# Kernel tuning notes

Hardware: AMD Instinct MI355X
Metric: run time of the kernel (lower is better)

Reference implementation:

```python
import jax, jax.numpy as jnp
import numpy as np

DIM = 1024
NUM_ATT = 8
NUM_HEADS = 16
HEAD_DIM = DIM // NUM_HEADS
ROPE_BASE = 10000.0
NEG_INF = -1e9


def _rope(x):
    # x: [B, H, L, hd]; torchtune-style interleaved RoPE applied along the sequence axis.
    B, H, L, hd = x.shape
    pos = jnp.arange(L, dtype=jnp.float32)
    inv_freq = 1.0 / (ROPE_BASE ** (jnp.arange(0, hd, 2, dtype=jnp.float32) / hd))
    ang = pos[:, None] * inv_freq[None, :]          # [L, hd/2]
    cos = jnp.cos(ang)[None, None]                  # [1,1,L,hd/2]
    sin = jnp.sin(ang)[None, None]
    xr = x.reshape(B, H, L, hd // 2, 2)
    x0, x1 = xr[..., 0], xr[..., 1]
    out = jnp.stack([x0 * cos - x1 * sin, x1 * cos + x0 * sin], axis=-1)
    return out.reshape(B, H, L, hd).astype(x.dtype)


def setup_inputs() -> dict:
    key = jax.random.key(0)
    ks = jax.random.split(key, 7)
    B, L = 32, 512
    x = jax.random.normal(ks[0], (B, L, DIM), dtype=jnp.float32)
    s = 0.02  # init scale for numerical sanity (init choice, not math)
    query_projs = jax.random.normal(ks[1], (NUM_ATT, DIM, DIM), dtype=jnp.float32) * s
    key_projs = jax.random.normal(ks[2], (NUM_ATT, DIM, DIM), dtype=jnp.float32) * s
    value_projs = jax.random.normal(ks[3], (NUM_ATT, DIM, DIM), dtype=jnp.float32) * s
    out_projs = jax.random.normal(ks[4], (NUM_ATT, DIM, DIM), dtype=jnp.float32) * s
    router_w = jax.random.normal(ks[5], (DIM, NUM_ATT), dtype=jnp.float32) * s
    router_b = jnp.zeros((NUM_ATT,), dtype=jnp.float32)
    return {"x": x, "query_projs": query_projs, "key_projs": key_projs,
            "value_projs": value_projs, "out_projs": out_projs,
            "router_w": router_w, "router_b": router_b}


def reference(x, query_projs, key_projs, value_projs, out_projs, router_w, router_b):
    B, L, D = x.shape
    H, hd = NUM_HEADS, HEAD_DIM
    scale = hd ** -0.5

    # top-1 routing on mean-pooled tokens
    logits = x.mean(axis=1) @ router_w + router_b       # [B, E]
    attn_probs = jax.nn.softmax(logits, axis=-1)
    routes = jnp.argmax(attn_probs, axis=-1)            # [B] int

    # per-batch weight gather (the memory-bound irregular access) + bmm
    qw = query_projs[routes]                             # [B, D, D]
    kw = key_projs[routes]
    vw = value_projs[routes]
    q = jnp.einsum('bld,bde->ble', x, qw)
    k = jnp.einsum('bld,bde->ble', x, kw)
    v = jnp.einsum('bld,bde->ble', x, vw)

    q = q.reshape(B, L, H, hd).transpose(0, 2, 1, 3)     # [B,H,L,hd]
    k = k.reshape(B, L, H, hd).transpose(0, 2, 1, 3)
    v = v.reshape(B, L, H, hd).transpose(0, 2, 1, 3)

    q = _rope(q)
    k = _rope(k)

    scores = jnp.einsum('bhld,bhmd->bhlm', q, k) * scale  # [B,H,L,L]
    causal = jnp.triu(jnp.ones((L, L), dtype=bool), k=1)  # True above diag = masked
    scores = jnp.where(causal[None, None], NEG_INF, scores)
    attn = jax.nn.softmax(scores, axis=-1)
    out = jnp.einsum('bhlm,bhmd->bhld', attn, v)          # [B,H,L,hd]
    out = out.transpose(0, 2, 1, 3).reshape(B, L, D)

    ow = out_projs[routes]                                # [B, D, D]
    out = jnp.einsum('bld,bde->ble', out, ow)
    return out, attn_probs
```

## Files before the change

### kernel.cpp

```cpp
#include <hip/hip_runtime.h>


typedef __attribute__((ext_vector_type(8))) short bf16x8;
typedef __attribute__((ext_vector_type(4))) float f32x4;

typedef const __attribute__((address_space(1))) unsigned short* gas_t;
typedef __attribute__((address_space(3))) unsigned short* las_t;

#define OFF_PART   (0ull)
#define OFF_ROUTES (2ull << 20)
#define OFF_XB     (3ull << 20)
#define OFF_WT     (40ull << 20)
#define OFF_QKV    (112ull << 20)

__device__ __forceinline__ unsigned short f2bf(float f){
  unsigned int u = __float_as_uint(f);
  u += 0x7fffu + ((u >> 16) & 1u);
  return (unsigned short)(u >> 16);
}


__global__ void meanpool_kernel(const float* __restrict__ x, float* __restrict__ part,
                                unsigned short* __restrict__ xb){
  const int b = blockIdx.x, lc = blockIdx.y, t = threadIdx.x;
  const size_t base = ((size_t)b*512 + lc*32)*1024;
  const float* xs = x + base;
  unsigned short* xo = xb + base;
  float4 a = {0.f, 0.f, 0.f, 0.f};
  for (int l = 0; l < 32; ++l){
    const float4 v = *(const float4*)(xs + l*1024 + t*4);
    a.x += v.x; a.y += v.y; a.z += v.z; a.w += v.w;
    ushort4 pk;
    pk.x = f2bf(v.x); pk.y = f2bf(v.y); pk.z = f2bf(v.z); pk.w = f2bf(v.w);
    *(ushort4*)(xo + l*1024 + t*4) = pk;
  }
  *(float4*)(part + ((size_t)b*16 + lc)*1024 + t*4) = a;
}


__global__ void router_kernel(const float* __restrict__ part,
                              const float* __restrict__ rw,
                              const float* __restrict__ rbias,
                              float* __restrict__ probs,
                              int* __restrict__ routes){
  const int b = blockIdx.x, t = threadIdx.x;
  const int lane = t & 63, wave = t >> 6;
  __shared__ float wred[4][8];
  float p[8] = {0.f,0.f,0.f,0.f,0.f,0.f,0.f,0.f};
  #pragma unroll
  for (int k = 0; k < 4; ++k){
    const int d = t + k*256;
    float s = 0.f;
    #pragma unroll
    for (int lc = 0; lc < 16; ++lc)
      s += part[((size_t)b*16 + lc)*1024 + d];
    s *= (1.0f/512.0f);
    const float4 w0 = *(const float4*)(rw + d*8);
    const float4 w1 = *(const float4*)(rw + d*8 + 4);
    p[0] = fmaf(s, w0.x, p[0]); p[1] = fmaf(s, w0.y, p[1]);
    p[2] = fmaf(s, w0.z, p[2]); p[3] = fmaf(s, w0.w, p[3]);
    p[4] = fmaf(s, w1.x, p[4]); p[5] = fmaf(s, w1.y, p[5]);
    p[6] = fmaf(s, w1.z, p[6]); p[7] = fmaf(s, w1.w, p[7]);
  }
  #pragma unroll
  for (int off = 1; off < 64; off <<= 1)
    #pragma unroll
    for (int e = 0; e < 8; ++e)
      p[e] += __shfl_xor(p[e], off, 64);
  if (lane == 0){
    #pragma unroll
    for (int e = 0; e < 8; ++e) wred[wave][e] = p[e];
  }
  __syncthreads();
  if (t == 0){
    float lg[8], mx = -3e38f; int am = 0;
    #pragma unroll
    for (int e = 0; e < 8; ++e){
      lg[e] = wred[0][e] + wred[1][e] + wred[2][e] + wred[3][e] + rbias[e];
      if (lg[e] > mx){ mx = lg[e]; am = e; }
    }
    float sum = 0.f, ex[8];
    #pragma unroll
    for (int e = 0; e < 8; ++e){ ex[e] = __expf(lg[e] - mx); sum += ex[e]; }
    const float inv = 1.0f / sum;
    #pragma unroll
    for (int e = 0; e < 8; ++e) probs[b*8 + e] = ex[e] * inv;
    routes[b] = am;
  }
}


__global__ void wcast_kernel(const float* __restrict__ W, unsigned short* __restrict__ Wt){
  __shared__ float tile[64][65];
  const int mtx = blockIdx.z;
  const float* Wm = W + (size_t)mtx*1024*1024;
  unsigned short* Wo = Wt + (size_t)mtx*1024*1024;
  const int t = threadIdx.x;
  const int r = t >> 4;
  const int c4 = t & 15;
  const int gx = blockIdx.x*64, gy = blockIdx.y*64;
  #pragma unroll
  for (int k = 0; k < 4; ++k){
    const int rr = r + 16*k;
    const float4 v = *(const float4*)(Wm + (size_t)(gy + rr)*1024 + gx + c4*4);
    tile[rr][c4*4+0] = v.x; tile[rr][c4*4+1] = v.y;
    tile[rr][c4*4+2] = v.z; tile[rr][c4*4+3] = v.w;
  }
  __syncthreads();
  #pragma unroll
  for (int k = 0; k < 4; ++k){
    const int rr = r + 16*k;
    ushort4 pk;
    pk.x = f2bf(tile[c4*4+0][rr]); pk.y = f2bf(tile[c4*4+1][rr]);
    pk.z = f2bf(tile[c4*4+2][rr]); pk.w = f2bf(tile[c4*4+3][rr]);
    *(ushort4*)(Wo + (size_t)(gx + rr)*1024 + gy + c4*4) = pk;
  }
}


template<int MODE>
__global__ __launch_bounds__(512, 2) void gemm_kernel(
    const unsigned short* __restrict__ A,
    const unsigned short* __restrict__ Wt,
    const int* __restrict__ routes,
    unsigned short* __restrict__ qkvout,
    float* __restrict__ outf)
{
  __shared__ __align__(16) unsigned short As[2][256*64];
  __shared__ __align__(16) unsigned short Bs[2][256*64];

  const int f = blockIdx.x + blockIdx.y*8;
  const int CH = (MODE == 0) ? 96 : 32;
  const int wg = (f & 7)*CH + (f >> 3);
  const int slice = wg >> 3;
  const int tile  = wg & 7;
  const int m0 = (tile >> 2)*256;
  const int n0 = (tile & 3)*256;
  const int b = (MODE == 0) ? (slice/3) : slice;
  const int p = (MODE == 0) ? (slice - b*3) : 0;

  const int route = routes[b];
  const unsigned short* Ab = A + (size_t)b*512*1024;
  const unsigned short* Wb = Wt + (size_t)((MODE == 0) ? (p*8 + route) : route)*1024*1024;

  const int t = threadIdx.x;
  const int lane = t & 63;
  const int wave = t >> 6;
  const int wm = (wave >> 2)*128;
  const int wn = (wave & 3)*64;
  const int quad = lane >> 4;
  const int ln = lane & 15;

  const int srow = t >> 3;
  const int sch  = (t & 7) ^ (srow & 7);
  const unsigned short* gA0 = Ab + (size_t)(m0 + srow)*1024 + sch*8;
  const unsigned short* gB0 = Wb + (size_t)(n0 + srow)*1024 + sch*8;

  const int w8 = ln & 7;
  const int aO0 = (wm + ln)*64 + ((quad    ) ^ w8)*8;
  const int aO1 = (wm + ln)*64 + ((quad + 4) ^ w8)*8;
  const int bO0 = (wn + ln)*64 + ((quad    ) ^ w8)*8;
  const int bO1 = (wn + ln)*64 + ((quad + 4) ^ w8)*8;

  f32x4 acc[8][4] = {};
  bf16x8 a0[4][2], a1[4][2], b01[2][2], b23[2][2];

#define STAGE(c_, T_) do { \
    const size_t ko_ = (size_t)(T_)*64; \
    las_t dA_ = (las_t)(&As[c_][0]) + (size_t)t*8; \
    las_t dB_ = (las_t)(&Bs[c_][0]) + (size_t)t*8; \
    _Pragma("unroll") \
    for (int k_ = 0; k_ < 4; ++k_){ \
      __builtin_amdgcn_global_load_lds((gas_t)(gA0 + ko_ + (size_t)k_*65536), dA_ + k_*4096, 16, 0, 0); \
      __builtin_amdgcn_global_load_lds((gas_t)(gB0 + ko_ + (size_t)k_*65536), dB_ + k_*4096, 16, 0, 0); \
    } \
  } while (0)

#define RD(ptr_, off_) (*(const bf16x8*)((ptr_) + (off_)))
#define READ_F0(pA_, pB_) do { \
    _Pragma("unroll") for (int f_ = 0; f_ < 4; ++f_){ \
      a0[f_][0] = RD(pA_, aO0 + f_*1024); a0[f_][1] = RD(pA_, aO1 + f_*1024); } \
    _Pragma("unroll") for (int f_ = 0; f_ < 2; ++f_){ \
      b01[f_][0] = RD(pB_, bO0 + f_*1024); b01[f_][1] = RD(pB_, bO1 + f_*1024); } \
  } while (0)
#define READ_F1(pA_) do { \
    _Pragma("unroll") for (int f_ = 0; f_ < 4; ++f_){ \
      a1[f_][0] = RD(pA_, aO0 + (4+f_)*1024); a1[f_][1] = RD(pA_, aO1 + (4+f_)*1024); } \
  } while (0)
#define READ_F2(pB_) do { \
    _Pragma("unroll") for (int f_ = 0; f_ < 2; ++f_){ \
      b23[f_][0] = RD(pB_, bO0 + (2+f_)*1024); b23[f_][1] = RD(pB_, bO1 + (2+f_)*1024); } \
  } while (0)

#define MSET(AF_, BF_, IB_, JB_) do { \
    _Pragma("unroll") for (int f_ = 0; f_ < 4; ++f_) \
    _Pragma("unroll") for (int n_ = 0; n_ < 2; ++n_) \
    _Pragma("unroll") for (int k_ = 0; k_ < 2; ++k_) \
      acc[IB_+f_][JB_+n_] = __builtin_amdgcn_mfma_f32_16x16x32_bf16( \
          AF_[f_][k_], BF_[n_][k_], acc[IB_+f_][JB_+n_], 0, 0, 0); \
  } while (0)

  STAGE(0, 0);
  STAGE(1, 1);
  asm volatile("s_waitcnt vmcnt(8)" ::: "memory");
  __builtin_amdgcn_s_barrier();
  READ_F0((&As[0][0]), (&Bs[0][0]));

  for (int g = 0; g < 16; ++g){
    const int c = g & 1;
    const unsigned short* pA  = &As[c][0];
    const unsigned short* pB  = &Bs[c][0];
    const unsigned short* pAn = &As[c ^ 1][0];
    const unsigned short* pBn = &Bs[c ^ 1][0];

    READ_F1(pA);
    __builtin_amdgcn_s_barrier();
    asm volatile("s_waitcnt lgkmcnt(8)" ::: "memory");
    __builtin_amdgcn_sched_barrier(0);
    __builtin_amdgcn_s_setprio(1);
    MSET(a0, b01, 0, 0);
    __builtin_amdgcn_s_setprio(0);
    __builtin_amdgcn_s_barrier();

    READ_F2(pB);
    __builtin_amdgcn_s_barrier();
    asm volatile("s_waitcnt lgkmcnt(4)" ::: "memory");
    __builtin_amdgcn_sched_barrier(0);
    __builtin_amdgcn_s_setprio(1);
    MSET(a1, b01, 4, 0);
    __builtin_amdgcn_s_setprio(0);
    __builtin_amdgcn_s_barrier();

    asm volatile("s_waitcnt lgkmcnt(0)" ::: "memory");
    __builtin_amdgcn_sched_barrier(0);
    __builtin_amdgcn_s_setprio(1);
    MSET(a1, b23, 4, 2);
    __builtin_amdgcn_s_setprio(0);
    __builtin_amdgcn_s_barrier();

    if (g < 14){
      STAGE(c, g + 2);
      asm volatile("s_waitcnt vmcnt(8)" ::: "memory");
    } else if (g == 14){
      asm volatile("s_waitcnt vmcnt(0)" ::: "memory");
    }
    __builtin_amdgcn_s_barrier();
    __builtin_amdgcn_s_setprio(1);
    MSET(a0, b23, 0, 2);
    __builtin_amdgcn_s_setprio(0);
    if (g < 15) READ_F0(pAn, pBn);
    __builtin_amdgcn_s_barrier();
  }
#undef STAGE
#undef RD
#undef READ_F0
#undef READ_F1
#undef READ_F2
#undef MSET

  if (MODE == 0){
    const size_t PSZ = (size_t)32*16*512*64;
    if (p < 2){
      #pragma unroll
      for (int fn = 0; fn < 4; ++fn){
        const int e  = n0 + wn + fn*16 + ln;
        const int h  = e >> 6;
        const int eh = e & 63;
        const float invf = exp2f(-0.41524101f * (float)(eh >> 1));
        float s1, c1; __sincosf(invf, &s1, &c1);
        unsigned short* outp = qkvout + ((((size_t)p*32 + b)*16 + h)*512)*64 + eh;
        #pragma unroll
        for (int fm = 0; fm < 8; ++fm){
          const int l0 = m0 + wm + fm*16 + quad*4;
          float sn, cs;
          __sincosf((float)l0 * invf, &sn, &cs);
          #pragma unroll
          for (int r = 0; r < 4; ++r){
            const int l = l0 + r;
            const float own = acc[fm][fn][r];
            const float par = __shfl_xor(own, 1, 64);
            const float v = (e & 1) ? fmaf(own, cs, par*sn) : fmaf(own, cs, -par*sn);
            outp[(size_t)l*64] = f2bf(v);
            const float nc = cs*c1 - sn*s1;
            const float ns = sn*c1 + cs*s1;
            cs = nc; sn = ns;
          }
        }
      }
    } else {
      #pragma unroll
      for (int fn = 0; fn < 4; ++fn){
        const int e  = n0 + wn + fn*16 + ln;
        const int h  = e >> 6;
        const int eh = e & 63;
        unsigned short* outp = qkvout + 2*PSZ + (((size_t)b*16 + h)*64 + eh)*512;
        #pragma unroll
        for (int fm = 0; fm < 8; ++fm){
          const int l0 = m0 + wm + fm*16 + quad*4;
          ushort4 pk;
          pk.x = f2bf(acc[fm][fn][0]); pk.y = f2bf(acc[fm][fn][1]);
          pk.z = f2bf(acc[fm][fn][2]); pk.w = f2bf(acc[fm][fn][3]);
          *(ushort4*)(outp + l0) = pk;
        }
      }
    }
  } else {
    #pragma unroll
    for (int fn = 0; fn < 4; ++fn){
      const int e = n0 + wn + fn*16 + ln;
      #pragma unroll
      for (int fm = 0; fm < 8; ++fm){
        #pragma unroll
        for (int r = 0; r < 4; ++r){
          const int l = m0 + wm + fm*16 + quad*4 + r;
          outf[((size_t)b*512 + l)*1024 + e] = acc[fm][fn][r];
        }
      }
    }
  }
}


#define PSTR 72

__global__ __launch_bounds__(256, 3) void attn_kernel(
    const unsigned short* __restrict__ qkv,
    unsigned short* __restrict__ ctx)
{
  __shared__ __align__(16) unsigned short Ks[2][64*64];
  __shared__ __align__(16) unsigned short Vts[2][64*64];
  __shared__ __align__(16) unsigned short Ps[4][32*PSTR];

  int wg = blockIdx.x + (blockIdx.y << 2) + (blockIdx.z << 6);
  wg = (wg & 7) * 256 + (wg >> 3);
  const int b  = wg >> 6;
  const int h  = (wg >> 2) & 15;
  const int qt = wg & 3;

  const size_t HO  = (((size_t)b)*16 + h)*512*64;
  const size_t PSZ = (size_t)32*16*512*64;
  const unsigned short* Qg  = qkv + HO;
  const unsigned short* Kg  = qkv + PSZ + HO;
  const unsigned short* Vtg = qkv + 2*PSZ + HO;

  const int t    = threadIdx.x;
  const int lane = t & 63;
  const int wave = t >> 6;
  const int quad = lane >> 4;
  const int ln   = lane & 15;

  const int u0 = t, u1 = t + 256;
  const int kr0 = u0 >> 3, kc0 = (u0 & 7) ^ (kr0 & 7);
  const int kr1 = u1 >> 3, kc1 = (u1 & 7) ^ (kr1 & 7);

  bf16x8 aq[2][2];
  #pragma unroll
  for (int rg = 0; rg < 2; ++rg){
    const int row = qt*128 + rg*64 + wave*16 + ln;
    #pragma unroll
    for (int ks = 0; ks < 2; ++ks)
      aq[rg][ks] = *(const bf16x8*)(Qg + (size_t)row*64 + ks*32 + quad*8);
  }

  const int ktEnd = 2*qt + 1;

  __builtin_amdgcn_global_load_lds((gas_t)(Kg  + kr0*64  + kc0*8), (las_t)(Ks[0]  + u0*8), 16,0,0);
  __builtin_amdgcn_global_load_lds((gas_t)(Kg  + kr1*64  + kc1*8), (las_t)(Ks[0]  + u1*8), 16,0,0);
  __builtin_amdgcn_global_load_lds((gas_t)(Vtg + kr0*512 + kc0*8), (las_t)(Vts[0] + u0*8), 16,0,0);
  __builtin_amdgcn_global_load_lds((gas_t)(Vtg + kr1*512 + kc1*8), (las_t)(Vts[0] + u1*8), 16,0,0);

  float m_r[2][4], l_r[2][4];
  #pragma unroll
  for (int rg = 0; rg < 2; ++rg)
    #pragma unroll
    for (int r = 0; r < 4; ++r){ m_r[rg][r] = -3e38f; l_r[rg][r] = 0.f; }
  f32x4 o[2][4] = {};

  const int swzl = ln & 7;
  unsigned short* Pw = Ps[wave];
  const int rowoff = wave*16 + quad*4;

  for (int kt = 0; kt <= ktEnd; ++kt){
    __syncthreads();
    if (kt < ktEnd){
      const unsigned short* Kn  = Kg + (kt+1)*4096;
      const int col = (kt+1)*64;
      unsigned short* kb = Ks[(kt+1)&1];
      unsigned short* vb = Vts[(kt+1)&1];
      __builtin_amdgcn_global_load_lds((gas_t)(Kn  + kr0*64 + kc0*8),        (las_t)(kb + u0*8), 16,0,0);
      __builtin_amdgcn_global_load_lds((gas_t)(Kn  + kr1*64 + kc1*8),        (las_t)(kb + u1*8), 16,0,0);
      __builtin_amdgcn_global_load_lds((gas_t)(Vtg + kr0*512 + col + kc0*8), (las_t)(vb + u0*8), 16,0,0);
      __builtin_amdgcn_global_load_lds((gas_t)(Vtg + kr1*512 + col + kc1*8), (las_t)(vb + u1*8), 16,0,0);
    }
    const unsigned short* ks_ = Ks[kt&1];
    const unsigned short* vt_ = Vts[kt&1];

    #pragma unroll
    for (int rg = 0; rg < 2; ++rg){
      if (rg == 0 && kt > 2*qt) continue;
      const bool diag = (kt == 2*qt + rg);

      f32x4 s[4] = {};
      __builtin_amdgcn_s_setprio(1);
      #pragma unroll
      for (int ks2 = 0; ks2 < 2; ++ks2){
        #pragma unroll
        for (int kn = 0; kn < 4; ++kn){
          const bf16x8 bk = *(const bf16x8*)(ks_ + (kn*16+ln)*64 + (((quad + ks2*4) ^ swzl))*8);
          s[kn] = __builtin_amdgcn_mfma_f32_16x16x32_bf16(aq[rg][ks2], bk, s[kn], 0, 0, 0);
        }
      }
      __builtin_amdgcn_s_setprio(0);

      float p[4][4], lm[4] = {-3e38f,-3e38f,-3e38f,-3e38f};
      #pragma unroll
      for (int kn = 0; kn < 4; ++kn){
        const int col = kn*16 + ln;
        #pragma unroll
        for (int r = 0; r < 4; ++r){
          float v = s[kn][r] * 0.125f;
          if (diag && col > rowoff + r) v = -1e9f;
          p[kn][r] = v;
          lm[r] = fmaxf(lm[r], v);
        }
      }
      #pragma unroll
      for (int off = 1; off < 16; off <<= 1)
        #pragma unroll
        for (int r = 0; r < 4; ++r)
          lm[r] = fmaxf(lm[r], __shfl_xor(lm[r], off, 64));
      float alpha[4], rsum[4];
      #pragma unroll
      for (int r = 0; r < 4; ++r){
        const float mn = fmaxf(m_r[rg][r], lm[r]);
        alpha[r] = __expf(m_r[rg][r] - mn);
        m_r[rg][r] = mn;
      }
      #pragma unroll
      for (int kn = 0; kn < 4; ++kn)
        #pragma unroll
        for (int r = 0; r < 4; ++r)
          p[kn][r] = __expf(p[kn][r] - m_r[rg][r]);
      #pragma unroll
      for (int r = 0; r < 4; ++r)
        rsum[r] = (p[0][r] + p[1][r]) + (p[2][r] + p[3][r]);
      #pragma unroll
      for (int off = 1; off < 16; off <<= 1)
        #pragma unroll
        for (int r = 0; r < 4; ++r)
          rsum[r] += __shfl_xor(rsum[r], off, 64);
      #pragma unroll
      for (int r = 0; r < 4; ++r) l_r[rg][r] = l_r[rg][r]*alpha[r] + rsum[r];
      #pragma unroll
      for (int dn = 0; dn < 4; ++dn)
        #pragma unroll
        for (int r = 0; r < 4; ++r)
          o[rg][dn][r] *= alpha[r];

      #pragma unroll
      for (int kn = 0; kn < 4; ++kn)
        #pragma unroll
        for (int r = 0; r < 4; ++r)
          Pw[(rg*16 + quad*4 + r)*PSTR + kn*16 + ln] = f2bf(p[kn][r]);

      __builtin_amdgcn_s_setprio(1);
      #pragma unroll
      for (int ks2 = 0; ks2 < 2; ++ks2){
        const bf16x8 ap = *(const bf16x8*)(Pw + (rg*16 + ln)*PSTR + quad*8 + ks2*32);
        #pragma unroll
        for (int dn = 0; dn < 4; ++dn){
          const bf16x8 bv = *(const bf16x8*)(vt_ + (dn*16+ln)*64 + (((quad + ks2*4) ^ swzl))*8);
          o[rg][dn] = __builtin_amdgcn_mfma_f32_16x16x32_bf16(ap, bv, o[rg][dn], 0, 0, 0);
        }
      }
      __builtin_amdgcn_s_setprio(0);
    }
  }

  #pragma unroll
  for (int rg = 0; rg < 2; ++rg){
    #pragma unroll
    for (int r = 0; r < 4; ++r){
      const float inv = 1.0f / l_r[rg][r];
      const int row = qt*128 + rg*64 + wave*16 + quad*4 + r;
      unsigned short* op = ctx + ((size_t)b*512 + row)*1024 + h*64 + ln;
      #pragma unroll
      for (int dn = 0; dn < 4; ++dn)
        op[dn*16] = f2bf(o[rg][dn][r] * inv);
    }
  }
}


extern "C" void kernel_launch(void* const* d_in, const int* in_sizes, int n_in,
                              void* d_out, int out_size, void* d_ws, size_t ws_size,
                              hipStream_t stream) {
  const float* x     = (const float*)d_in[0];
  const float* qw    = (const float*)d_in[1];
  const float* kw    = (const float*)d_in[2];
  const float* vw    = (const float*)d_in[3];
  const float* ow    = (const float*)d_in[4];
  const float* rw    = (const float*)d_in[5];
  const float* rbias = (const float*)d_in[6];
  float* out = (float*)d_out;
  char* ws = (char*)d_ws;

  float* part            = (float*)(ws + OFF_PART);
  int* routes            = (int*)(ws + OFF_ROUTES);
  unsigned short* xb     = (unsigned short*)(ws + OFF_XB);
  unsigned short* wt     = (unsigned short*)(ws + OFF_WT);
  unsigned short* qkvbuf = (unsigned short*)(ws + OFF_QKV);
  unsigned short* ctx    = xb;
  float* probs = out + (size_t)32*512*1024;

  meanpool_kernel<<<dim3(32, 16), 256, 0, stream>>>(x, part, xb);
  router_kernel<<<32, 256, 0, stream>>>(part, rw, rbias, probs, routes);
  wcast_kernel<<<dim3(16, 16, 8), 256, 0, stream>>>(qw, wt);
  wcast_kernel<<<dim3(16, 16, 8), 256, 0, stream>>>(kw, wt + (size_t)8*1024*1024);
  wcast_kernel<<<dim3(16, 16, 8), 256, 0, stream>>>(vw, wt + (size_t)16*1024*1024);
  wcast_kernel<<<dim3(16, 16, 8), 256, 0, stream>>>(ow, wt + (size_t)24*1024*1024);
  gemm_kernel<0><<<dim3(8, 96), 512, 0, stream>>>(xb, wt, routes, qkvbuf, nullptr);
  attn_kernel<<<dim3(4, 16, 32), 256, 0, stream>>>(qkvbuf, ctx);
  gemm_kernel<1><<<dim3(8, 32), 512, 0, stream>>>(ctx, wt + (size_t)24*1024*1024, routes,
                                                  nullptr, out);
}
```

Before: 513.6 us.

## Permute GEMM B-tile columns so each lane owns four adjacent outputs for vector stores

Remaps which output columns each lane's MFMA fragments cover, so a lane holds four consecutive columns (ln*4+fn) instead of columns strided by 16. The B-tile LDS swizzle and read offsets change to match. The epilogues can then apply RoPE pairs within one thread without cross-lane shuffles, and can write packed ushort4 and float4 stores instead of scalar strided ones. The cost is a different LDS bank-conflict pattern on B reads, which needs the new swizzle to stay conflict-free.

```diff
diff --git a/kernel.cpp b/kernel.cpp
--- a/kernel.cpp
+++ b/kernel.cpp
@@ -152,15 +152,16 @@
   const int ln = lane & 15;
 
   const int srow = t >> 3;
-  const int sch  = (t & 7) ^ (srow & 7);
-  const unsigned short* gA0 = Ab + (size_t)(m0 + srow)*1024 + sch*8;
-  const unsigned short* gB0 = Wb + (size_t)(n0 + srow)*1024 + sch*8;
+  const int schA = (t & 7) ^ (srow & 7);
+  const int schB = (t & 7) ^ ((t >> 5) & 7);
+  const unsigned short* gA0 = Ab + (size_t)(m0 + srow)*1024 + schA*8;
+  const unsigned short* gB0 = Wb + (size_t)(n0 + srow)*1024 + schB*8;
 
   const int w8 = ln & 7;
   const int aO0 = (wm + ln)*64 + ((quad    ) ^ w8)*8;
   const int aO1 = (wm + ln)*64 + ((quad + 4) ^ w8)*8;
-  const int bO0 = (wn + ln)*64 + ((quad    ) ^ w8)*8;
-  const int bO1 = (wn + ln)*64 + ((quad + 4) ^ w8)*8;
+  const int bO0 = (wn + ln*4)*64 + ((quad    ) ^ w8)*8;
+  const int bO1 = (wn + ln*4)*64 + ((quad + 4) ^ w8)*8;
 
   f32x4 acc[8][4] = {};
   bf16x8 a0[4][2], a1[4][2], b01[2][2], b23[2][2];
@@ -181,7 +182,7 @@
     _Pragma("unroll") for (int f_ = 0; f_ < 4; ++f_){ \
       a0[f_][0] = RD(pA_, aO0 + f_*1024); a0[f_][1] = RD(pA_, aO1 + f_*1024); } \
     _Pragma("unroll") for (int f_ = 0; f_ < 2; ++f_){ \
-      b01[f_][0] = RD(pB_, bO0 + f_*1024); b01[f_][1] = RD(pB_, bO1 + f_*1024); } \
+      b01[f_][0] = RD(pB_, bO0 + f_*64); b01[f_][1] = RD(pB_, bO1 + f_*64); } \
   } while (0)
 #define READ_F1(pA_) do { \
     _Pragma("unroll") for (int f_ = 0; f_ < 4; ++f_){ \
@@ -189,7 +190,7 @@
   } while (0)
 #define READ_F2(pB_) do { \
     _Pragma("unroll") for (int f_ = 0; f_ < 2; ++f_){ \
-      b23[f_][0] = RD(pB_, bO0 + (2+f_)*1024); b23[f_][1] = RD(pB_, bO1 + (2+f_)*1024); } \
+      b23[f_][0] = RD(pB_, bO0 + (2+f_)*64); b23[f_][1] = RD(pB_, bO1 + (2+f_)*64); } \
   } while (0)
 
 #define MSET(AF_, BF_, IB_, JB_) do { \
@@ -260,39 +261,41 @@
 
   if (MODE == 0){
     const size_t PSZ = (size_t)32*16*512*64;
+    const int h = (n0 + wn) >> 6;
     if (p < 2){
+      const int eh0 = ln*4;
+      const float invf0 = exp2f(-0.41524101f * (float)(ln*2));
+      const float invf1 = invf0 * 0.74989420832f;
+      float sc0, cc0, sc1, cc1;
+      __sincosf(invf0, &sc0, &cc0);
+      __sincosf(invf1, &sc1, &cc1);
+      unsigned short* outp = qkvout + ((((size_t)p*32 + b)*16 + h)*512)*64 + eh0;
+      #pragma unroll
+      for (int fm = 0; fm < 8; ++fm){
+        const int l0 = m0 + wm + fm*16 + quad*4;
+        float s0, c0, s1, c1;
+        __sincosf((float)l0 * invf0, &s0, &c0);
+        __sincosf((float)l0 * invf1, &s1, &c1);
+        #pragma unroll
+        for (int r = 0; r < 4; ++r){
+          const int l = l0 + r;
+          const float x0 = acc[fm][0][r], x1 = acc[fm][1][r];
+          const float x2 = acc[fm][2][r], x3 = acc[fm][3][r];
+          ushort4 pk;
+          pk.x = f2bf(x0*c0 - x1*s0);
+          pk.y = f2bf(x1*c0 + x0*s0);
+          pk.z = f2bf(x2*c1 - x3*s1);
+          pk.w = f2bf(x3*c1 + x2*s1);
+          *(ushort4*)(outp + (size_t)l*64) = pk;
+          const float nc0 = c0*cc0 - s0*sc0, ns0 = s0*cc0 + c0*sc0;
+          const float nc1 = c1*cc1 - s1*sc1, ns1 = s1*cc1 + c1*sc1;
+          c0 = nc0; s0 = ns0; c1 = nc1; s1 = ns1;
+        }
+      }
+    } else {
       #pragma unroll
       for (int fn = 0; fn < 4; ++fn){
-        const int e  = n0 + wn + fn*16 + ln;
-        const int h  = e >> 6;
-        const int eh = e & 63;
-        const float invf = exp2f(-0.41524101f * (float)(eh >> 1));
-        float s1, c1; __sincosf(invf, &s1, &c1);
-        unsigned short* outp = qkvout + ((((size_t)p*32 + b)*16 + h)*512)*64 + eh;
-        #pragma unroll
-        for (int fm = 0; fm < 8; ++fm){
-          const int l0 = m0 + wm + fm*16 + quad*4;
-          float sn, cs;
-          __sincosf((float)l0 * invf, &sn, &cs);
-          #pragma unroll
-          for (int r = 0; r < 4; ++r){
-            const int l = l0 + r;
-            const float own = acc[fm][fn][r];
-            const float par = __shfl_xor(own, 1, 64);
-            const float v = (e & 1) ? fmaf(own, cs, par*sn) : fmaf(own, cs, -par*sn);
-            outp[(size_t)l*64] = f2bf(v);
-            const float nc = cs*c1 - sn*s1;
-            const float ns = sn*c1 + cs*s1;
-            cs = nc; sn = ns;
-          }
-        }
-      }
-    } else {
-      #pragma unroll
-      for (int fn = 0; fn < 4; ++fn){
-        const int e  = n0 + wn + fn*16 + ln;
-        const int h  = e >> 6;
-        const int eh = e & 63;
+        const int eh = ln*4 + fn;
         unsigned short* outp = qkvout + 2*PSZ + (((size_t)b*16 + h)*64 + eh)*512;
         #pragma unroll
         for (int fm = 0; fm < 8; ++fm){
@@ -305,16 +308,16 @@
       }
     }
   } else {
-    #pragma unroll
-    for (int fn = 0; fn < 4; ++fn){
-      const int e = n0 + wn + fn*16 + ln;
-      #pragma unroll
-      for (int fm = 0; fm < 8; ++fm){
-        #pragma unroll
-        for (int r = 0; r < 4; ++r){
-          const int l = m0 + wm + fm*16 + quad*4 + r;
-          outf[((size_t)b*512 + l)*1024 + e] = acc[fm][fn][r];
-        }
+    const int e0 = n0 + wn + ln*4;
+    #pragma unroll
+    for (int fm = 0; fm < 8; ++fm){
+      #pragma unroll
+      for (int r = 0; r < 4; ++r){
+        const int l = m0 + wm + fm*16 + quad*4 + r;
+        float4 f4;
+        f4.x = acc[fm][0][r]; f4.y = acc[fm][1][r];
+        f4.z = acc[fm][2][r]; f4.w = acc[fm][3][r];
+        *(float4*)(outf + ((size_t)b*512 + l)*1024 + e0) = f4;
       }
     }
   }
```

Measured after the change: 509.9 us. About the same (-0.7%).
